# Kernel tuning notes

Measured on AMD Instinct MI355X. Metric: run time of the kernel, lower is better.

Reference implementation:

```python
import jax, jax.numpy as jnp
import numpy as np
import math

H, KV, D, HID, WIN = 8, 4, 256, 2048, 1024  # heads, kv heads, head_dim, hidden, sliding window
B, S = 1, 2048

def _rms(x, scale):
    # Gemma3RMSNorm: hardcoded 1e-6 eps, (1+scale) gain
    var = jnp.mean(jnp.square(x), axis=-1, keepdims=True)
    return x * jax.lax.rsqrt(var + 1e-6) * (1.0 + scale)

def _rot_half(x):
    x1, x2 = jnp.split(x, 2, axis=-1)
    return jnp.concatenate((-x2, x1), axis=-1)

def setup_inputs() -> dict:
    key = jax.random.key(0)
    ks = jax.random.split(key, 8)
    x = jax.random.normal(ks[0], (B, S, HID), jnp.float32)
    attn_mask = jnp.ones((B, S), jnp.bool_)
    segment_pos = jnp.broadcast_to(jnp.arange(S, dtype=jnp.int32)[None], (B, S))
    # true RoPE tables, theta=1e6 (Gemma3 global layers)
    inv_freq = 1.0 / (1e6 ** (np.arange(0, D, 2, dtype=np.float32) / D))
    ang = np.arange(S, dtype=np.float32)[:, None] * inv_freq[None, :]  # [S, D/2]
    emb = np.concatenate([ang, ang], axis=-1)                          # [S, D]
    cos = jnp.asarray(np.cos(emb), jnp.float32)[None]                  # [1, S, D]
    sin = jnp.asarray(np.sin(emb), jnp.float32)[None]
    sd = 1.0 / math.sqrt(HID)
    wq = jax.random.normal(ks[1], (HID, H * D), jnp.float32) * sd
    wk = jax.random.normal(ks[2], (HID, KV * D), jnp.float32) * sd
    wv = jax.random.normal(ks[3], (HID, KV * D), jnp.float32) * sd
    wo = jax.random.normal(ks[4], (H * D, HID), jnp.float32) * (1.0 / math.sqrt(H * D))
    q_scale = jnp.zeros((D,), jnp.float32)  # zeros_init as in module
    k_scale = jnp.zeros((D,), jnp.float32)
    return dict(x=x, attn_mask=attn_mask, segment_pos=segment_pos, cos=cos, sin=sin,
                wq=wq, wk=wk, wv=wv, wo=wo, q_scale=q_scale, k_scale=k_scale)

def reference(x, attn_mask, segment_pos, cos, sin, wq, wk, wv, wo, q_scale, k_scale):
    b, s, _ = x.shape
    # projections -> [b, h, s, d]
    q = (x @ wq).reshape(b, s, H, D).transpose(0, 2, 1, 3)
    k = (x @ wk).reshape(b, s, KV, D).transpose(0, 2, 1, 3)
    v = (x @ wv).reshape(b, s, KV, D).transpose(0, 2, 1, 3)
    # per-head QK RMSNorm
    q = _rms(q, q_scale)
    k = _rms(k, k_scale)
    # RoPE (cos/sin broadcast over head axis, unsqueeze_dim=1)
    c, sn = cos[:, None], sin[:, None]
    q = q * c + _rot_half(q) * sn
    k = k * c + _rot_half(k) * sn
    # GQA: repeat-interleave kv heads
    rep = H // KV
    k = jnp.repeat(k, rep, axis=1)
    v = jnp.repeat(v, rep, axis=1)
    scores = jnp.einsum('bhqd,bhkd->bhqk', q, k) / math.sqrt(D)
    # causal + padding mask (q_len > 1 path, no image bidirectional mask)
    causal = jnp.tril(jnp.ones((s, s), jnp.bool_))
    mask = causal[None] & attn_mask[:, None, :]          # [b, q, kv]
    # sliding window mask (prefill: cache positions = arange)
    kvpos = jnp.arange(s)
    pos = segment_pos[:, :, None]
    sliding = (kvpos[None, None] > pos - WIN) & (kvpos[None, None] < pos + WIN)
    full = mask & sliding
    scores = scores + jnp.where(full[:, None], 0.0, -1e37)
    w = jax.nn.softmax(scores.astype(jnp.float32), axis=-1).astype(scores.dtype)
    out = jnp.einsum('bhqk,bhkd->bhqd', w, v)
    out = out.transpose(0, 2, 1, 3).reshape(b, s, H * D)
    return out @ wo
```

## Files before the change

kernel.cpp:

```cpp
#include <hip/hip_runtime.h>
#include <hip/hip_bf16.h>

#define S_LEN 2048
#define HID 2048
#define NH 8
#define NKV 4
#define HD 256
#define WIN 1024

typedef __hip_bfloat16 bf16;
typedef __attribute__((ext_vector_type(8))) short bf16x8;
typedef __attribute__((ext_vector_type(4))) float f32x4;

__device__ __forceinline__ void gld_lds16(void* lds, const void* g) {
    __builtin_amdgcn_global_load_lds(
        (const __attribute__((address_space(1))) unsigned int*)g,
        (__attribute__((address_space(3))) unsigned int*)lds,
        16, 0, 0);
}


__device__ __forceinline__ void transT_body(const float* __restrict__ src, bf16* __restrict__ dst,
                                            int R, int C, int r0, int c0) {
    __shared__ bf16 Ts[64][72];
    const int tid = threadIdx.x;
    {
        const int r = tid >> 2;
        const int cq = (tid & 3) * 16;
#pragma unroll
        for (int j = 0; j < 16; j += 4) {
            float4 v = *(const float4*)&src[(size_t)(r0 + r) * C + c0 + cq + j];
            Ts[cq + j + 0][r] = __float2bfloat16(v.x);
            Ts[cq + j + 1][r] = __float2bfloat16(v.y);
            Ts[cq + j + 2][r] = __float2bfloat16(v.z);
            Ts[cq + j + 3][r] = __float2bfloat16(v.w);
        }
    }
    __syncthreads();
    {
        const int c = tid >> 2;
        const int rq = (tid & 3) * 16;
#pragma unroll
        for (int j = 0; j < 16; j += 8)
            *(uint4*)&dst[(size_t)(c0 + c) * R + r0 + rq + j] = *(const uint4*)&Ts[c][rq + j];
    }
}

__global__ __launch_bounds__(256)
void prep_all(const float* __restrict__ xf, const float* __restrict__ wqf,
              const float* __restrict__ wkf, const float* __restrict__ wvf,
              const float* __restrict__ wof,
              bf16* __restrict__ xb, bf16* __restrict__ wqkvt, bf16* __restrict__ wot) {
    const int bid = blockIdx.x;
    if (bid < 2048) {
        const int i = bid * 256 + threadIdx.x;
        float4 a = ((const float4*)xf)[i * 2];
        float4 b = ((const float4*)xf)[i * 2 + 1];
        union { uint4 v; bf16 h[8]; } u;
        u.h[0] = __float2bfloat16(a.x); u.h[1] = __float2bfloat16(a.y);
        u.h[2] = __float2bfloat16(a.z); u.h[3] = __float2bfloat16(a.w);
        u.h[4] = __float2bfloat16(b.x); u.h[5] = __float2bfloat16(b.y);
        u.h[6] = __float2bfloat16(b.z); u.h[7] = __float2bfloat16(b.w);
        ((uint4*)xb)[i] = u.v;
    } else if (bid < 4096) {
        const int t = bid - 2048;
        const int bx = t & 63, by = t >> 6;
        const float* src; int C, c0, drow0;
        if (bx < 32)      { src = wqf; C = 2048; c0 = bx * 64;        drow0 = bx * 64; }
        else if (bx < 48) { src = wkf; C = 1024; c0 = (bx - 32) * 64; drow0 = 2048 + (bx - 32) * 64; }
        else              { src = wvf; C = 1024; c0 = (bx - 48) * 64; drow0 = 3072 + (bx - 48) * 64; }
        bf16* dshift = wqkvt + ((size_t)drow0 - c0) * HID;
        transT_body(src, dshift, HID, C, by * 64, c0);
    } else {
        const int t = bid - 4096;
        const int bx = t & 31, by = t >> 5;
        transT_body(wof, wot, NH * HD, HID, by * 64, bx * 64);
    }
}

template<int MODE>
__global__ __launch_bounds__(256)
void gemm_m97d(const bf16* __restrict__ A, const bf16* __restrict__ Bt,
               bf16* __restrict__ Cb,
               bf16* __restrict__ Qo, bf16* __restrict__ Ko, bf16* __restrict__ Vto,
               int N, int K, int KS) {
    __shared__ bf16 As[2][128][32];
    __shared__ bf16 Bs[2][128][32];
    const int tid = threadIdx.x;
    const int w = tid >> 6, lane = tid & 63;
    const int lnm = lane & 15, quad = lane >> 4;
    const int wm = (w & 1) * 64, wn = (w >> 1) * 64;
    const int m0 = blockIdx.y * 128, n0 = blockIdx.x * 128;
    const int kbeg = (MODE == 2) ? blockIdx.z * KS : 0;
    const int nk = ((MODE == 2) ? KS : K) / 32;

    const int lr = lane >> 2;
    const int lc = (lane & 3) * 8;

    f32x4 acc[4][4];
#pragma unroll
    for (int i = 0; i < 4; ++i)
#pragma unroll
        for (int j = 0; j < 4; ++j) acc[i][j] = (f32x4){0.f, 0.f, 0.f, 0.f};

    const bf16* ga0 = A  + (size_t)(m0 + 32 * w + lr) * K + kbeg + lc;
    const bf16* ga1 = ga0 + (size_t)16 * K;
    const bf16* gb0 = Bt + (size_t)(n0 + 32 * w + lr) * K + kbeg + lc;
    const bf16* gb1 = gb0 + (size_t)16 * K;

    gld_lds16(&As[0][32 * w][0],      ga0);
    gld_lds16(&As[0][32 * w + 16][0], ga1);
    gld_lds16(&Bs[0][32 * w][0],      gb0);
    gld_lds16(&Bs[0][32 * w + 16][0], gb1);

    int cur = 0;
    for (int i = 0; i < nk; ++i) {
        __syncthreads();
        if (i + 1 < nk) {
            const int ko = (i + 1) * 32;
            gld_lds16(&As[cur ^ 1][32 * w][0],      ga0 + ko);
            gld_lds16(&As[cur ^ 1][32 * w + 16][0], ga1 + ko);
            gld_lds16(&Bs[cur ^ 1][32 * w][0],      gb0 + ko);
            gld_lds16(&Bs[cur ^ 1][32 * w + 16][0], gb1 + ko);
        }
        bf16x8 af[4], bfr[4];
#pragma unroll
        for (int t = 0; t < 4; ++t) {
            af[t]  = *(const bf16x8*)&As[cur][wm + t * 16 + lnm][quad * 8];
            bfr[t] = *(const bf16x8*)&Bs[cur][wn + t * 16 + lnm][quad * 8];
        }
#pragma unroll
        for (int tm = 0; tm < 4; ++tm)
#pragma unroll
            for (int tn = 0; tn < 4; ++tn)
                acc[tm][tn] = __builtin_amdgcn_mfma_f32_16x16x32_bf16(
                    af[tm], bfr[tn], acc[tm][tn], 0, 0, 0);
        cur ^= 1;
    }

#pragma unroll
    for (int tm = 0; tm < 4; ++tm)
#pragma unroll
        for (int tn = 0; tn < 4; ++tn)
#pragma unroll
            for (int r = 0; r < 4; ++r) {
                const int row = m0 + wm + tm * 16 + quad * 4 + r;
                const int col = n0 + wn + tn * 16 + lnm;
                const float v = acc[tm][tn][r];
                if constexpr (MODE == 2) {
                    Cb[(size_t)blockIdx.z * 2048 * 2048 + (size_t)row * N + col] =
                        __float2bfloat16(v);
                } else {
                    if (col < 2048)
                        Qo[(size_t)row * (NH * HD) + col] = __float2bfloat16(v);
                    else if (col < 3072)
                        Ko[(size_t)row * (NKV * HD) + col - 2048] = __float2bfloat16(v);
                    else
                        Vto[(size_t)(col - 3072) * S_LEN + row] = __float2bfloat16(v);
                }
            }
}

__global__ __launch_bounds__(256)
void splitk_add(const bf16* __restrict__ p, float* __restrict__ out) {
    const int i = blockIdx.x * 256 + threadIdx.x;
    union { uint4 v; bf16 h[8]; } a, b;
    a.v = ((const uint4*)p)[i];
    b.v = ((const uint4*)(p + (size_t)2048 * 2048))[i];
    float4 o0, o1;
    o0.x = (float)a.h[0] + (float)b.h[0]; o0.y = (float)a.h[1] + (float)b.h[1];
    o0.z = (float)a.h[2] + (float)b.h[2]; o0.w = (float)a.h[3] + (float)b.h[3];
    o1.x = (float)a.h[4] + (float)b.h[4]; o1.y = (float)a.h[5] + (float)b.h[5];
    o1.z = (float)a.h[6] + (float)b.h[6]; o1.w = (float)a.h[7] + (float)b.h[7];
    ((float4*)out)[i * 2]     = o0;
    ((float4*)out)[i * 2 + 1] = o1;
}

__global__ __launch_bounds__(64)
void rmsrope_kernel(bf16* __restrict__ Q, bf16* __restrict__ Kb,
                    const float* __restrict__ cosb, const float* __restrict__ sinb,
                    const float* __restrict__ qscale, const float* __restrict__ kscale,
                    float qmul) {
    const int p = blockIdx.x;
    const int hg = blockIdx.y;
    const int lane = threadIdx.x;

    bf16* base;
    const float* scale;
    float mul;
    if (hg < NH) { base = Q + (size_t)p * (NH * HD) + hg * HD; scale = qscale; mul = qmul; }
    else         { base = Kb + (size_t)p * (NKV * HD) + (hg - NH) * HD; scale = kscale; mul = 1.f; }

    const int d0 = lane * 2;
    float x0 = (float)base[d0],       x1 = (float)base[d0 + 1];
    float y0 = (float)base[d0 + 128], y1 = (float)base[d0 + 129];

    float ss = x0 * x0 + x1 * x1 + y0 * y0 + y1 * y1;
#pragma unroll
    for (int off = 32; off > 0; off >>= 1) ss += __shfl_xor(ss, off, 64);
    const float r = rsqrtf(ss * (1.0f / (float)HD) + 1e-6f);

    x0 *= r * (1.f + scale[d0]);
    x1 *= r * (1.f + scale[d0 + 1]);
    y0 *= r * (1.f + scale[d0 + 128]);
    y1 *= r * (1.f + scale[d0 + 129]);

    const size_t cb = (size_t)p * HD;
    const float c0 = cosb[cb + d0],       c1 = cosb[cb + d0 + 1];
    const float cA = cosb[cb + d0 + 128], cB = cosb[cb + d0 + 129];
    const float s0 = sinb[cb + d0],       s1 = sinb[cb + d0 + 1];
    const float sA = sinb[cb + d0 + 128], sB = sinb[cb + d0 + 129];

    base[d0]       = __float2bfloat16((x0 * c0 - y0 * s0) * mul);
    base[d0 + 1]   = __float2bfloat16((x1 * c1 - y1 * s1) * mul);
    base[d0 + 128] = __float2bfloat16((y0 * cA + x0 * sA) * mul);
    base[d0 + 129] = __float2bfloat16((y1 * cB + x1 * sB) * mul);
}

#define NCHUNK 4
__global__ __launch_bounds__(256)
void attn_mfma(const bf16* __restrict__ Q, const bf16* __restrict__ K,
               const bf16* __restrict__ Vt, bf16* __restrict__ Op,
               float2* __restrict__ ml) {
    __shared__ bf16 Ks[32][264];
    __shared__ bf16 Vs[256][40];
    __shared__ bf16 Pl[4][16][40];
    const int qt = blockIdx.x, h = blockIdx.y, chunk = blockIdx.z, kvh = h >> 1;
    const int tid = threadIdx.x, w = tid >> 6, lane = tid & 63;
    const int lnm = lane & 15, quad = lane >> 4;

    bf16x8 qf[8];
    const int qrow = qt * 64 + w * 16 + lnm;
#pragma unroll
    for (int s = 0; s < 8; ++s)
        qf[s] = *(const bf16x8*)&Q[(size_t)qrow * HID + h * HD + s * 32 + quad * 8];

    f32x4 o[16];
#pragma unroll
    for (int i = 0; i < 16; ++i) o[i] = (f32x4){0.f, 0.f, 0.f, 0.f};
    float M[4] = {-3e38f, -3e38f, -3e38f, -3e38f};
    float L[4] = {0.f, 0.f, 0.f, 0.f};

    const int ktlo = (qt >= 16) ? (2 * qt - 32) : 0;
    const int kthi = 2 * qt + 1;
    const int ntile = kthi - ktlo + 1;
    const int c0 = ktlo + (chunk * ntile) / NCHUNK;
    const int c1 = ktlo + ((chunk + 1) * ntile) / NCHUNK - 1;

    for (int kt = c0; kt <= c1; ++kt) {
#pragma unroll
        for (int p = 0; p < 4; ++p) {
            const int row = p * 8 + (tid >> 5);
            const int d8 = (tid & 31) * 8;
            *(uint4*)&Ks[row][d8] =
                *(const uint4*)&K[(size_t)(kt * 32 + row) * (NKV * HD) + kvh * HD + d8];
        }
#pragma unroll
        for (int p = 0; p < 4; ++p) {
            const int d = p * 64 + (tid >> 2);
            const int c8 = (tid & 3) * 8;
            *(uint4*)&Vs[d][c8] =
                *(const uint4*)&Vt[(size_t)(kvh * HD + d) * S_LEN + kt * 32 + c8];
        }
        __syncthreads();

        f32x4 s4[2];
        s4[0] = (f32x4){0.f, 0.f, 0.f, 0.f};
        s4[1] = (f32x4){0.f, 0.f, 0.f, 0.f};
#pragma unroll
        for (int t = 0; t < 2; ++t)
#pragma unroll
            for (int s = 0; s < 8; ++s) {
                bf16x8 kf = *(const bf16x8*)&Ks[t * 16 + lnm][s * 32 + quad * 8];
                s4[t] = __builtin_amdgcn_mfma_f32_16x16x32_bf16(qf[s], kf, s4[t], 0, 0, 0);
            }
#pragma unroll
        for (int t = 0; t < 2; ++t)
#pragma unroll
            for (int r = 0; r < 4; ++r) {
                const int m_g = qt * 64 + w * 16 + quad * 4 + r;
                const int n_g = kt * 32 + t * 16 + lnm;
                if (n_g > m_g || n_g + (WIN - 1) < m_g) s4[t][r] = -1e30f;
            }
        float mx[4], rs[4], al[4];
#pragma unroll
        for (int r = 0; r < 4; ++r) {
            mx[r] = fmaxf(s4[0][r], s4[1][r]);
#pragma unroll
            for (int off = 1; off < 16; off <<= 1)
                mx[r] = fmaxf(mx[r], __shfl_xor(mx[r], off, 64));
            const float Mn = fmaxf(M[r], mx[r]);
            al[r] = __expf(M[r] - Mn);
            M[r] = Mn;
        }
#pragma unroll
        for (int t = 0; t < 2; ++t)
#pragma unroll
            for (int r = 0; r < 4; ++r)
                s4[t][r] = __expf(s4[t][r] - M[r]);
#pragma unroll
        for (int r = 0; r < 4; ++r) {
            rs[r] = s4[0][r] + s4[1][r];
#pragma unroll
            for (int off = 1; off < 16; off <<= 1)
                rs[r] += __shfl_xor(rs[r], off, 64);
            L[r] = L[r] * al[r] + rs[r];
        }
#pragma unroll
        for (int t2 = 0; t2 < 16; ++t2)
#pragma unroll
            for (int r = 0; r < 4; ++r) o[t2][r] *= al[r];
#pragma unroll
        for (int t = 0; t < 2; ++t)
#pragma unroll
            for (int r = 0; r < 4; ++r)
                Pl[w][quad * 4 + r][t * 16 + lnm] = __float2bfloat16(s4[t][r]);
        bf16x8 pa = *(const bf16x8*)&Pl[w][lnm][quad * 8];
#pragma unroll
        for (int t2 = 0; t2 < 16; ++t2) {
            bf16x8 vb = *(const bf16x8*)&Vs[t2 * 16 + lnm][quad * 8];
            o[t2] = __builtin_amdgcn_mfma_f32_16x16x32_bf16(pa, vb, o[t2], 0, 0, 0);
        }
        __syncthreads();
    }

    float rL[4];
#pragma unroll
    for (int r = 0; r < 4; ++r) rL[r] = (L[r] > 0.f) ? (1.f / L[r]) : 0.f;
    bf16* Opc = Op + (size_t)chunk * S_LEN * HID;
#pragma unroll
    for (int t2 = 0; t2 < 16; ++t2)
#pragma unroll
        for (int r = 0; r < 4; ++r)
            Opc[(size_t)(qt * 64 + w * 16 + quad * 4 + r) * HID + h * HD + t2 * 16 + lnm] =
                __float2bfloat16(o[t2][r] * rL[r]);
    if (lnm == 0) {
#pragma unroll
        for (int r = 0; r < 4; ++r) {
            const int row = qt * 64 + w * 16 + quad * 4 + r;
            ml[((size_t)chunk * S_LEN + row) * NH + h] = make_float2(M[r], L[r]);
        }
    }
}

__global__ __launch_bounds__(256)
void attn_combine(const bf16* __restrict__ Op, const float2* __restrict__ ml,
                  bf16* __restrict__ O) {
    const int row = blockIdx.x, h = blockIdx.y, d = threadIdx.x;
    float2 c[NCHUNK];
    float Mx = -3e38f;
#pragma unroll
    for (int i = 0; i < NCHUNK; ++i) {
        c[i] = ml[((size_t)i * S_LEN + row) * NH + h];
        Mx = fmaxf(Mx, c[i].x);
    }
    float wsum = 0.f, wgt[NCHUNK];
#pragma unroll
    for (int i = 0; i < NCHUNK; ++i) {
        wgt[i] = c[i].y * __expf(c[i].x - Mx);
        wsum += wgt[i];
    }
    const float inv = 1.0f / wsum;
    const size_t idx = (size_t)row * HID + h * HD + d;
    float acc = 0.f;
#pragma unroll
    for (int i = 0; i < NCHUNK; ++i)
        acc += wgt[i] * (float)Op[(size_t)i * S_LEN * HID + idx];
    O[idx] = __float2bfloat16(acc * inv);
}

extern "C" void kernel_launch(void* const* d_in, const int* in_sizes, int n_in,
                              void* d_out, int out_size, void* d_ws, size_t ws_size,
                              hipStream_t stream) {
    const float* xf   = (const float*)d_in[0];
    const float* cosb = (const float*)d_in[3];
    const float* sinb = (const float*)d_in[4];
    const float* wqf  = (const float*)d_in[5];
    const float* wkf  = (const float*)d_in[6];
    const float* wvf  = (const float*)d_in[7];
    const float* wof  = (const float*)d_in[8];
    const float* qs   = (const float*)d_in[9];
    const float* ks   = (const float*)d_in[10];
    float* out = (float*)d_out;
    char* ws = (char*)d_ws;

    bf16*   wot   = (bf16*)(ws);
    bf16*   Qb    = (bf16*)(ws + ( 8ull << 20));
    bf16*   Kb    = (bf16*)(ws + (16ull << 20));
    bf16*   Vtb   = (bf16*)(ws + (20ull << 20));
    bf16*   wqkvt = (bf16*)(ws + (24ull << 20));
    bf16*   xb    = (bf16*)(ws + (40ull << 20));
    bf16*   Op    = (bf16*)(ws + (24ull << 20));
    bf16*   Ab    = (bf16*)(ws + (40ull << 20));
    bf16*   pk    = (bf16*)(ws + (24ull << 20));
    float2* ml    = (float2*)(ws + (56ull << 20));

    dim3 blk(256);

    prep_all<<<5120, blk, 0, stream>>>(xf, wqf, wkf, wvf, wof, xb, wqkvt, wot);

    gemm_m97d<1><<<dim3(32, 16), blk, 0, stream>>>(
        xb, wqkvt, nullptr, Qb, Kb, Vtb, 4096, HID, 0);

    rmsrope_kernel<<<dim3(S_LEN, NH + NKV), dim3(64), 0, stream>>>(
        Qb, Kb, cosb, sinb, qs, ks, 0.0625f);

    attn_mfma<<<dim3(S_LEN / 64, NH, NCHUNK), blk, 0, stream>>>(Qb, Kb, Vtb, Op, ml);
    attn_combine<<<dim3(S_LEN, NH), blk, 0, stream>>>(Op, ml, Ab);

    gemm_m97d<2><<<dim3(16, 16, 2), blk, 0, stream>>>(
        Ab, wot, pk, nullptr, nullptr, nullptr, HID, HID, 1024);
    splitk_add<<<2048, blk, 0, stream>>>(pk, out);
}
```

Before: 294.7 us.

## Rewrite projection GEMMs with 8-wave 256x128 tiles and triple-buffered swizzled LDS

Replaces the 128x128, 4-wave, double-buffered GEMM with a 512-thread kernel that computes 256x128 tiles over a 64-deep K step. It adds a three-stage LDS ring fed by global_load_lds, an XOR-swizzled LDS layout to avoid bank conflicts, and split barriers with s_setprio around the MFMA bursts. Blocks are mapped to XCDs so that tiles sharing operands land on the same chiplet, which aims to improve L2 reuse and keep matrix cores busy. In exchange it needs 144KB of dynamic shared memory with a one-time attribute setup, and it hardcodes K=2048 and the grid shapes.

```diff
diff --git a/kernel.cpp b/kernel.cpp
--- a/kernel.cpp
+++ b/kernel.cpp
@@ -79,23 +79,53 @@
 }
 
 template<int MODE>
-__global__ __launch_bounds__(256)
-void gemm_m97d(const bf16* __restrict__ A, const bf16* __restrict__ Bt,
-               bf16* __restrict__ Cb,
-               bf16* __restrict__ Qo, bf16* __restrict__ Ko, bf16* __restrict__ Vto,
-               int N, int K, int KS) {
-    __shared__ bf16 As[2][128][32];
-    __shared__ bf16 Bs[2][128][32];
+__global__ __launch_bounds__(512, 2)
+void gemm8p(const bf16* __restrict__ A, const bf16* __restrict__ Bt,
+            bf16* __restrict__ Cb,
+            bf16* __restrict__ Qo, bf16* __restrict__ Ko, bf16* __restrict__ Vto) {
+    extern __shared__ bf16 smem[];
+    bf16* AsP = smem;
+    bf16* BsP = smem + 3 * 256 * 64;
+
     const int tid = threadIdx.x;
     const int w = tid >> 6, lane = tid & 63;
     const int lnm = lane & 15, quad = lane >> 4;
-    const int wm = (w & 1) * 64, wn = (w >> 1) * 64;
-    const int m0 = blockIdx.y * 128, n0 = blockIdx.x * 128;
-    const int kbeg = (MODE == 2) ? blockIdx.z * KS : 0;
-    const int nk = ((MODE == 2) ? KS : K) / 32;
-
-    const int lr = lane >> 2;
-    const int lc = (lane & 3) * 8;
+    const int wr = w >> 1, wc = w & 1;
+    const int r8 = lane >> 3;
+    const int swz = ((lane & 7) ^ r8) * 8;
+
+    const int bid = blockIdx.x;
+    const int xcd = bid & 7, idx = bid >> 3;
+    int m0, n0, kbeg, nt;
+    size_t zoff = 0;
+    if constexpr (MODE == 1) {
+        const int m_t = (xcd >> 2) * 4 + (idx >> 3);
+        const int n_t = (xcd & 3) * 8 + (idx & 7);
+        m0 = m_t * 256; n0 = n_t * 128; kbeg = 0; nt = 2048 / 64;
+    } else {
+        const int z   = xcd >> 2;
+        const int n_t = (xcd & 3) * 4 + (idx & 3);
+        const int m_t = idx >> 2;
+        m0 = m_t * 256; n0 = n_t * 128; kbeg = z * 1024; nt = 1024 / 64;
+        zoff = (size_t)z * 2048 * 2048;
+    }
+    const int K = 2048;
+
+    const bf16* pA[4];
+#pragma unroll
+    for (int g = 0; g < 4; ++g)
+        pA[g] = A + (size_t)(m0 + w * 32 + g * 8 + r8) * K + kbeg + swz;
+    const bf16* pB[2];
+#pragma unroll
+    for (int g = 0; g < 2; ++g)
+        pB[g] = Bt + (size_t)(n0 + w * 16 + g * 8 + r8) * K + kbeg + swz;
+    const int dA = w * 32 * 64;
+    const int dB = w * 16 * 64;
+
+#define STG_A(slot, g, t) gld_lds16(AsP + (slot) * 16384 + dA + (g) * 512, pA[g] + (t) * 64)
+#define STG_B(slot, g, t) gld_lds16(BsP + (slot) * 8192  + dB + (g) * 512, pB[g] + (t) * 64)
+#define LDFRAG(base, row, kh) \
+    (*(const bf16x8*)((base) + (row) * 64 + (((((kh) << 2) | quad) ^ ((row) & 7)) << 3)))
 
     f32x4 acc[4][4];
 #pragma unroll
@@ -103,40 +133,78 @@
 #pragma unroll
         for (int j = 0; j < 4; ++j) acc[i][j] = (f32x4){0.f, 0.f, 0.f, 0.f};
 
-    const bf16* ga0 = A  + (size_t)(m0 + 32 * w + lr) * K + kbeg + lc;
-    const bf16* ga1 = ga0 + (size_t)16 * K;
-    const bf16* gb0 = Bt + (size_t)(n0 + 32 * w + lr) * K + kbeg + lc;
-    const bf16* gb1 = gb0 + (size_t)16 * K;
-
-    gld_lds16(&As[0][32 * w][0],      ga0);
-    gld_lds16(&As[0][32 * w + 16][0], ga1);
-    gld_lds16(&Bs[0][32 * w][0],      gb0);
-    gld_lds16(&Bs[0][32 * w + 16][0], gb1);
-
-    int cur = 0;
-    for (int i = 0; i < nk; ++i) {
-        __syncthreads();
-        if (i + 1 < nk) {
-            const int ko = (i + 1) * 32;
-            gld_lds16(&As[cur ^ 1][32 * w][0],      ga0 + ko);
-            gld_lds16(&As[cur ^ 1][32 * w + 16][0], ga1 + ko);
-            gld_lds16(&Bs[cur ^ 1][32 * w][0],      gb0 + ko);
-            gld_lds16(&Bs[cur ^ 1][32 * w + 16][0], gb1 + ko);
-        }
-        bf16x8 af[4], bfr[4];
-#pragma unroll
-        for (int t = 0; t < 4; ++t) {
-            af[t]  = *(const bf16x8*)&As[cur][wm + t * 16 + lnm][quad * 8];
-            bfr[t] = *(const bf16x8*)&Bs[cur][wn + t * 16 + lnm][quad * 8];
-        }
-#pragma unroll
-        for (int tm = 0; tm < 4; ++tm)
-#pragma unroll
-            for (int tn = 0; tn < 4; ++tn)
-                acc[tm][tn] = __builtin_amdgcn_mfma_f32_16x16x32_bf16(
-                    af[tm], bfr[tn], acc[tm][tn], 0, 0, 0);
-        cur ^= 1;
-    }
+    STG_A(0, 0, 0); STG_A(0, 1, 0); STG_A(0, 2, 0); STG_A(0, 3, 0);
+    STG_B(0, 0, 0); STG_B(0, 1, 0);
+    STG_A(1, 0, 1); STG_A(1, 1, 1); STG_A(1, 2, 1); STG_A(1, 3, 1);
+    STG_B(1, 0, 1); STG_B(1, 1, 1);
+    asm volatile("s_waitcnt vmcnt(6)" ::: "memory");
+    __builtin_amdgcn_sched_barrier(0);
+    __builtin_amdgcn_s_barrier();
+
+    int sc = 0;
+    for (int t = 0; t < nt; ++t) {
+        const int ss = (sc == 0) ? 2 : sc - 1;
+        const bf16* As_ = AsP + sc * 16384;
+        const bf16* Bs_ = BsP + sc * 8192;
+        const bool pf = (t + 2 < nt);
+
+        bf16x8 a0[2][2], b[4][2];
+#pragma unroll
+        for (int tm = 0; tm < 2; ++tm)
+#pragma unroll
+            for (int kh = 0; kh < 2; ++kh)
+                a0[tm][kh] = LDFRAG(As_, wr * 64 + tm * 16 + lnm, kh);
+#pragma unroll
+        for (int tn = 0; tn < 4; ++tn)
+#pragma unroll
+            for (int kh = 0; kh < 2; ++kh)
+                b[tn][kh] = LDFRAG(Bs_, wc * 64 + tn * 16 + lnm, kh);
+        if (pf) { STG_A(ss, 0, t + 2); STG_A(ss, 1, t + 2); STG_B(ss, 0, t + 2); }
+        __builtin_amdgcn_s_barrier();
+        asm volatile("s_waitcnt lgkmcnt(0)" ::: "memory");
+        __builtin_amdgcn_sched_barrier(0);
+        __builtin_amdgcn_s_setprio(1);
+#pragma unroll
+        for (int kh = 0; kh < 2; ++kh)
+#pragma unroll
+            for (int tm = 0; tm < 2; ++tm)
+#pragma unroll
+                for (int tn = 0; tn < 4; ++tn)
+                    acc[tm][tn] = __builtin_amdgcn_mfma_f32_16x16x32_bf16(
+                        a0[tm][kh], b[tn][kh], acc[tm][tn], 0, 0, 0);
+        __builtin_amdgcn_s_setprio(0);
+        __builtin_amdgcn_s_barrier();
+
+        bf16x8 a1[2][2];
+#pragma unroll
+        for (int tm = 0; tm < 2; ++tm)
+#pragma unroll
+            for (int kh = 0; kh < 2; ++kh)
+                a1[tm][kh] = LDFRAG(As_, wr * 64 + (tm + 2) * 16 + lnm, kh);
+        if (pf) { STG_A(ss, 2, t + 2); STG_A(ss, 3, t + 2); STG_B(ss, 1, t + 2); }
+        if (pf) { asm volatile("s_waitcnt vmcnt(6)" ::: "memory"); }
+        else    { asm volatile("s_waitcnt vmcnt(0)" ::: "memory"); }
+        __builtin_amdgcn_sched_barrier(0);
+        __builtin_amdgcn_s_barrier();
+        asm volatile("s_waitcnt lgkmcnt(0)" ::: "memory");
+        __builtin_amdgcn_sched_barrier(0);
+        __builtin_amdgcn_s_setprio(1);
+#pragma unroll
+        for (int kh = 0; kh < 2; ++kh)
+#pragma unroll
+            for (int tm = 0; tm < 2; ++tm)
+#pragma unroll
+                for (int tn = 0; tn < 4; ++tn)
+                    acc[tm + 2][tn] = __builtin_amdgcn_mfma_f32_16x16x32_bf16(
+                        a1[tm][kh], b[tn][kh], acc[tm + 2][tn], 0, 0, 0);
+        __builtin_amdgcn_s_setprio(0);
+        __builtin_amdgcn_s_barrier();
+
+        sc = (sc == 2) ? 0 : sc + 1;
+    }
+#undef STG_A
+#undef STG_B
+#undef LDFRAG
 
 #pragma unroll
     for (int tm = 0; tm < 4; ++tm)
@@ -144,12 +212,11 @@
         for (int tn = 0; tn < 4; ++tn)
 #pragma unroll
             for (int r = 0; r < 4; ++r) {
-                const int row = m0 + wm + tm * 16 + quad * 4 + r;
-                const int col = n0 + wn + tn * 16 + lnm;
+                const int row = m0 + wr * 64 + tm * 16 + quad * 4 + r;
+                const int col = n0 + wc * 64 + tn * 16 + lnm;
                 const float v = acc[tm][tn][r];
                 if constexpr (MODE == 2) {
-                    Cb[(size_t)blockIdx.z * 2048 * 2048 + (size_t)row * N + col] =
-                        __float2bfloat16(v);
+                    Cb[zoff + (size_t)row * 2048 + col] = __float2bfloat16(v);
                 } else {
                     if (col < 2048)
                         Qo[(size_t)row * (NH * HD) + col] = __float2bfloat16(v);
@@ -397,10 +464,19 @@
 
     dim3 blk(256);
 
+    static bool attr_done = false;
+    if (!attr_done) {
+        (void)hipFuncSetAttribute(reinterpret_cast<const void*>(gemm8p<1>),
+                                  hipFuncAttributeMaxDynamicSharedMemorySize, 147456);
+        (void)hipFuncSetAttribute(reinterpret_cast<const void*>(gemm8p<2>),
+                                  hipFuncAttributeMaxDynamicSharedMemorySize, 147456);
+        attr_done = true;
+    }
+
     prep_all<<<5120, blk, 0, stream>>>(xf, wqf, wkf, wvf, wof, xb, wqkvt, wot);
 
-    gemm_m97d<1><<<dim3(32, 16), blk, 0, stream>>>(
-        xb, wqkvt, nullptr, Qb, Kb, Vtb, 4096, HID, 0);
+    gemm8p<1><<<dim3(256), dim3(512), 147456, stream>>>(
+        xb, wqkvt, nullptr, Qb, Kb, Vtb);
 
     rmsrope_kernel<<<dim3(S_LEN, NH + NKV), dim3(64), 0, stream>>>(
         Qb, Kb, cosb, sinb, qs, ks, 0.0625f);
@@ -408,7 +484,7 @@
     attn_mfma<<<dim3(S_LEN / 64, NH, NCHUNK), blk, 0, stream>>>(Qb, Kb, Vtb, Op, ml);
     attn_combine<<<dim3(S_LEN, NH), blk, 0, stream>>>(Op, ml, Ab);
 
-    gemm_m97d<2><<<dim3(16, 16, 2), blk, 0, stream>>>(
-        Ab, wot, pk, nullptr, nullptr, nullptr, HID, HID, 1024);
+    gemm8p<2><<<dim3(256), dim3(512), 147456, stream>>>(
+        Ab, wot, pk, nullptr, nullptr, nullptr);
     splitk_add<<<2048, blk, 0, stream>>>(pk, out);
 }
```

New measurement: 275.4 us. -6.5%, faster.
